# Kernel tuning notes

Measured on AMD Instinct MI355X. Metric: run time of the kernel, lower is better.

The kernel has to match this reference:

```python
import jax, jax.numpy as jnp
import numpy as np
from jax import lax

DIM = 192
HEADS = 6
WS = 8
SHIFT = 4
RED = max(8, DIM // 8)  # 24
HID = 4 * DIM


def _rel_index(ws):
    coords = np.stack(np.meshgrid(np.arange(ws), np.arange(ws), indexing='ij'))  # [2,ws,ws]
    flat = coords.reshape(2, -1)
    rel = (flat[:, :, None] - flat[:, None, :]).transpose(1, 2, 0)  # [T,T,2]
    rel[:, :, 0] += ws - 1
    rel[:, :, 1] += ws - 1
    rel[:, :, 0] *= 2 * ws - 1
    return rel.sum(-1)  # [T,T]


def _build_mask(h, w, ws, shift):
    img = np.zeros((h, w))
    slices = (slice(0, -ws), slice(-ws, -shift), slice(-shift, None))
    cnt = 0
    for hs in slices:
        for wcs in slices:
            img[hs, wcs] = cnt
            cnt += 1
    mw = img.reshape(h // ws, ws, w // ws, ws).transpose(0, 2, 1, 3).reshape(-1, ws * ws)
    diff = mw[:, None, :] - mw[:, :, None]  # [nW,T,T], diff[w,i,j]=mw[w,j]-mw[w,i]
    return np.where(diff != 0, -100.0, 0.0).astype(np.float32)


def _ln(x, g, b):
    m = x.mean(-1, keepdims=True)
    v = ((x - m) ** 2).mean(-1, keepdims=True)
    return (x - m) / jnp.sqrt(v + 1e-5) * g + b


def _conv(x, k, b, pad):
    y = lax.conv_general_dilated(x, k, (1, 1), [(pad, pad), (pad, pad)],
                                 dimension_numbers=('NCHW', 'OIHW', 'NCHW'))
    return y + b[None, :, None, None]


def setup_inputs() -> dict:
    key = jax.random.key(0)
    ks = jax.random.split(key, 16)
    rn = lambda k, s, sc=0.02: jax.random.normal(k, s, dtype=jnp.float32) * sc
    C = DIM
    return {
        'x': jax.random.normal(ks[0], (4, 256 * 256, C), dtype=jnp.float32),
        'ln1_g': jnp.ones((C,), jnp.float32), 'ln1_b': jnp.zeros((C,), jnp.float32),
        'w_qkv': rn(ks[1], (3 * C, C)), 'b_qkv': jnp.zeros((3 * C,), jnp.float32),
        'rel_table': rn(ks[2], ((2 * WS - 1) ** 2, HEADS)),
        'w_proj': rn(ks[3], (C, C)), 'b_proj': jnp.zeros((C,), jnp.float32),
        'ln2_g': jnp.ones((C,), jnp.float32), 'ln2_b': jnp.zeros((C,), jnp.float32),
        'w_fc1': rn(ks[4], (HID, C)), 'b_fc1': jnp.zeros((HID,), jnp.float32),
        'w_fc2': rn(ks[5], (C, HID)), 'b_fc2': jnp.zeros((C,), jnp.float32),
        'conv1_w': rn(ks[6], (RED, C, 1, 1)), 'conv1_b': jnp.zeros((RED,), jnp.float32),
        'conv2_w': rn(ks[7], (RED, RED, 3, 3)), 'conv2_b': jnp.zeros((RED,), jnp.float32),
        'conv3_w': rn(ks[8], (C, RED, 1, 1)), 'conv3_b': jnp.zeros((C,), jnp.float32),
        'se_w1': rn(ks[9], (RED, C)), 'se_w2': rn(ks[10], (C, RED)),
        'h': 256, 'w': 256,
    }


def reference(x, ln1_g, ln1_b, w_qkv, b_qkv, rel_table, w_proj, b_proj,
              ln2_g, ln2_b, w_fc1, b_fc1, w_fc2, b_fc2,
              conv1_w, conv1_b, conv2_w, conv2_b, conv3_w, conv3_b,
              se_w1, se_w2, h, w):
    B, _, C = x.shape
    ws, T, nh = WS, WS * WS, HEADS
    hd = C // nh
    scale = hd ** -0.5

    nx = _ln(x, ln1_g, ln1_b).reshape(B, h, w, C)
    local = nx.transpose(0, 3, 1, 2)  # NCHW for LCE

    # shifted window attention
    sh = jnp.roll(nx, (-SHIFT, -SHIFT), axis=(1, 2))
    win = sh.reshape(B, h // ws, ws, w // ws, ws, C).transpose(0, 1, 3, 2, 4, 5).reshape(-1, T, C)
    qkv = (win @ w_qkv.T + b_qkv).reshape(-1, T, 3, nh, hd).transpose(2, 0, 3, 1, 4)
    q, k, v = qkv[0] * scale, qkv[1], qkv[2]  # [BW, nh, T, hd]
    attn = jnp.einsum('whid,whjd->whij', q, k)  # [BW, nh, T, T]
    bias = rel_table[_rel_index(ws).reshape(-1)].reshape(T, T, nh).transpose(2, 0, 1)
    attn = attn + bias[None]
    mask = jnp.asarray(_build_mask(h, w, ws, SHIFT))  # [nW, T, T]
    nW = mask.shape[0]
    attn = attn.reshape(B, nW, nh, T, T) + mask[None, :, None]
    attn = jax.nn.softmax(attn, axis=-1).reshape(-1, nh, T, T)
    out = jnp.einsum('whij,whjd->whid', attn, v).transpose(0, 2, 1, 3).reshape(-1, T, C)
    out = out @ w_proj.T + b_proj
    out = out.reshape(B, h // ws, w // ws, ws, ws, C).transpose(0, 1, 3, 2, 4, 5).reshape(B, h, w, C)
    out = jnp.roll(out, (SHIFT, SHIFT), axis=(1, 2))

    x1 = x + out.reshape(B, h * w, C)
    n2 = _ln(x1, ln2_g, ln2_b)
    mlp = jax.nn.gelu(n2 @ w_fc1.T + b_fc1, approximate=False) @ w_fc2.T + b_fc2
    x2 = x1 + mlp

    # LocalContextExtractor (SE-style)
    y = _conv(local, conv1_w, conv1_b, 0)
    y = _conv(y, conv2_w, conv2_b, 1)
    y = _conv(y, conv3_w, conv3_b, 0)
    y = jnp.where(y >= 0, y, 0.2 * y)  # LeakyReLU(0.2)
    pooled = y.mean(axis=(2, 3))  # [B, C]
    wgt = jax.nn.sigmoid(jax.nn.relu(pooled @ se_w1.T) @ se_w2.T)
    y = y * wgt[:, :, None, None]
    lc = y.reshape(B, C, h * w).transpose(0, 2, 1)
    return x2 + lc
```

## Files before the change

kernel.cpp:

```cpp
#include <hip/hip_runtime.h>
#include <hip/hip_bf16.h>

typedef unsigned short u16;
typedef unsigned long long u64;
typedef __attribute__((ext_vector_type(8))) short short8x;
typedef __attribute__((ext_vector_type(4))) float f32x4;
typedef __bf16 bf16x8 __attribute__((ext_vector_type(8)));

#define SCALE 0.17677669529663687f

__device__ __forceinline__ u16 f2bf(float f) {
  unsigned u = __builtin_bit_cast(unsigned, f);
  unsigned r = (u + 0x7FFFu + ((u >> 16) & 1u)) >> 16;
  return (u16)r;
}
__device__ __forceinline__ float bf2f(u16 h) {
  return __builtin_bit_cast(float, ((unsigned)h) << 16);
}
__device__ __forceinline__ float gelu_f(float v) {
  float t = v * v;
  float a = __builtin_fmaf(t, -0.07135481627f, -1.59576912161f);
  float e = __expf(v * a);
  return v * __builtin_amdgcn_rcpf(1.0f + e);
}
__device__ __forceinline__ int swz(int row, int col, int ld) {
  return row * ld + ((((col >> 3) ^ (row & 7)) << 3) | (col & 7));
}
__device__ __forceinline__ short8x ldfrag(const u16* s, int row, int kb, int ld) {
  return *(const short8x*)(s + row * ld + (((kb >> 3) ^ (row & 7)) << 3));
}
__device__ __forceinline__ short8x ldg8(const u16* p) { return *(const short8x*)p; }

__device__ __forceinline__ f32x4 MFMA(short8x a, short8x b, f32x4 c) {
  return __builtin_amdgcn_mfma_f32_16x16x32_bf16(
      __builtin_bit_cast(bf16x8, a), __builtin_bit_cast(bf16x8, b), c, 0, 0, 0);
}
__device__ __forceinline__ u64 pack4(float a, float b, float c, float d) {
  return (u64)f2bf(a) | ((u64)f2bf(b) << 16) | ((u64)f2bf(c) << 32) | ((u64)f2bf(d) << 48);
}

__global__ void cvt_kernel(const float* __restrict__ wqkv, const float* __restrict__ wproj,
                           const float* __restrict__ wfc1, const float* __restrict__ wfc2,
                           const float* __restrict__ c1, const float* __restrict__ c3,
                           const float* __restrict__ c2,
                           u16* oq, u16* op, u16* o1, u16* o2, u16* oc1, u16* oc3,
                           float* ow2r) {
  int i = blockIdx.x * 256 + threadIdx.x;
  if (i < 110592) { float f = wqkv[i]; if (i < 36864) f *= SCALE; oq[i] = f2bf(f); return; }
  i -= 110592;
  if (i < 36864) { op[i] = f2bf(wproj[i]); return; }
  i -= 36864;
  if (i < 147456) { o1[i] = f2bf(wfc1[i]); return; }
  i -= 147456;
  if (i < 147456) { o2[i] = f2bf(wfc2[i]); return; }
  i -= 147456;
  if (i < 6144) { int r = i / 192, c = i - r * 192; oc1[i] = (r < 24) ? f2bf(c1[r * 192 + c]) : (u16)0; return; }
  i -= 6144;
  if (i < 6144) { int cc = i >> 5, k = i & 31; oc3[i] = (k < 24) ? f2bf(c3[cc * 24 + k]) : (u16)0; return; }
  i -= 6144;
  if (i < 5184) { int t = i / 576, rr = i - t * 576; int ci = rr / 24, co = rr - ci * 24;
                  ow2r[i] = c2[co * 216 + ci * 9 + t]; }
}

__global__ __launch_bounds__(256) void ln1_kernel(const float* __restrict__ x,
                                                  const float* __restrict__ g,
                                                  const float* __restrict__ b,
                                                  u16* __restrict__ nx) {
  const int wid = threadIdx.x >> 6, lane = threadIdx.x & 63;
  const int row = blockIdx.x * 4 + wid;
  const float* xr = x + row * 192;
  f32x4 v = {0.f, 0.f, 0.f, 0.f};
  if (lane < 48) v = *(const f32x4*)(xr + lane * 4);
  float s = v[0] + v[1] + v[2] + v[3];
  for (int m = 1; m < 64; m <<= 1) s += __shfl_xor(s, m);
  const float mean = s * (1.0f / 192.0f);
  f32x4 d;
#pragma unroll
  for (int r = 0; r < 4; ++r) d[r] = v[r] - mean;
  float q = (lane < 48) ? (d[0] * d[0] + d[1] * d[1] + d[2] * d[2] + d[3] * d[3]) : 0.f;
  for (int m = 1; m < 64; m <<= 1) q += __shfl_xor(q, m);
  const float rstd = rsqrtf(q * (1.0f / 192.0f) + 1e-5f);
  if (lane < 48) {
    const f32x4 gg = *(const f32x4*)(g + lane * 4);
    const f32x4 bb = *(const f32x4*)(b + lane * 4);
    u64 pk = pack4(d[0] * rstd * gg[0] + bb[0], d[1] * rstd * gg[1] + bb[1],
                   d[2] * rstd * gg[2] + bb[2], d[3] * rstd * gg[3] + bb[3]);
    *(u64*)(nx + row * 192 + lane * 4) = pk;
  }
}

__global__ __launch_bounds__(512, 4) void attn_kernel(
    const float* __restrict__ x, const u16* __restrict__ nx,
    const u16* __restrict__ wq, const float* __restrict__ bqkv,
    const float* __restrict__ rel, const u16* __restrict__ wp,
    const float* __restrict__ bproj, u16* __restrict__ vT,
    float* __restrict__ x1out) {
  __shared__ u16 sQK[64 * 384];
  __shared__ float sRel[1350];
  __shared__ int sG[64];

  const int tid = threadIdx.x, blk = blockIdx.x;
  const int b = blk >> 10, wi = (blk >> 5) & 31, wj = blk & 31;
  const int wv = tid >> 6, lane = tid & 63, lr = lane & 15, hi = lane >> 4;
  u16* vTw = vT + blk * 12288;

  for (int i = tid; i < 1350; i += 512) sRel[i] = rel[i];
  if (tid < 64) {
    int si = (wi * 8 + (tid >> 3) + 4) & 255, sj = (wj * 8 + (tid & 7) + 4) & 255;
    sG[tid] = b * 65536 + si * 256 + sj;
  }
  for (int i = tid; i < 64 * 96; i += 512) {
    int r = i / 96, w32 = i - r * 96;
    int si = (wi * 8 + (r >> 3) + 4) & 255, sj = (wj * 8 + (r & 7) + 4) & 255;
    int grow = b * 65536 + si * 256 + sj;
    unsigned v = ((const unsigned*)nx)[grow * 96 + w32];
    ((unsigned*)sQK)[r * 192 + ((((w32 >> 2) ^ (r & 7)) << 2) | (w32 & 3))] = v;
  }
  __syncthreads();

  f32x4 acc[4][4] = {};
  if (wv < 6) {
    const int wbase = wv * 64;
#pragma unroll
    for (int kk = 0; kk < 6; ++kk) {
      short8x Xf[4];
#pragma unroll
      for (int tt = 0; tt < 4; ++tt) Xf[tt] = ldfrag(sQK, tt * 16 + lr, kk * 32 + hi * 8, 384);
#pragma unroll
      for (int wt = 0; wt < 4; ++wt) {
        short8x Wf = ldg8(wq + (wbase + wt * 16 + lr) * 192 + kk * 32 + hi * 8);
#pragma unroll
        for (int tt = 0; tt < 4; ++tt) acc[wt][tt] = MFMA(Wf, Xf[tt], acc[wt][tt]);
      }
    }
  } else {
    const int vbase = (wv - 6) * 96;
#pragma unroll
    for (int half = 0; half < 2; ++half) {
      short8x Bf[3][6];
      float bv[3];
#pragma unroll
      for (int j = 0; j < 3; ++j) {
        const int vc = vbase + (half * 3 + j) * 16 + lr;
#pragma unroll
        for (int kk = 0; kk < 6; ++kk)
          Bf[j][kk] = ldg8(wq + (384 + vc) * 192 + kk * 32 + hi * 8);
        bv[j] = bqkv[384 + vc];
      }
#pragma unroll
      for (int mt = 0; mt < 4; ++mt) {
        f32x4 vacc[3] = {};
#pragma unroll
        for (int kk = 0; kk < 6; ++kk) {
          short8x A = ldfrag(sQK, mt * 16 + lr, kk * 32 + hi * 8, 384);
#pragma unroll
          for (int j = 0; j < 3; ++j) vacc[j] = MFMA(A, Bf[j][kk], vacc[j]);
        }
#pragma unroll
        for (int j = 0; j < 3; ++j) {
          u64 pk = pack4(vacc[j][0] + bv[j], vacc[j][1] + bv[j],
                         vacc[j][2] + bv[j], vacc[j][3] + bv[j]);
          *(u64*)(vTw + (vbase + (half * 3 + j) * 16 + lr) * 64 + mt * 16 + hi * 4) = pk;
        }
      }
    }
  }
  __syncthreads();

  if (wv < 6) {
    const int wbase = wv * 64;
#pragma unroll
    for (int wt = 0; wt < 4; ++wt) {
      const int oc0 = wbase + wt * 16 + hi * 4;
      const f32x4 bq = *(const f32x4*)(bqkv + oc0);
      const float sc = (oc0 < 192) ? SCALE : 1.0f;
#pragma unroll
      for (int tt = 0; tt < 4; ++tt) {
        u64 pk = pack4(acc[wt][tt][0] + bq[0] * sc, acc[wt][tt][1] + bq[1] * sc,
                       acc[wt][tt][2] + bq[2] * sc, acc[wt][tt][3] + bq[3] * sc);
        *(u64*)&sQK[swz(tt * 16 + lr, oc0, 384)] = pk;
      }
    }
  }
  __syncthreads();

  f32x4 S[3][4];
#pragma unroll
  for (int i = 0; i < 3; ++i) {
    const int s = wv + 8 * i, h3 = s >> 2, q = s & 3;
    short8x Aq = ldfrag(sQK, q * 16 + lr, h3 * 32 + hi * 8, 384);
#pragma unroll
    for (int nt = 0; nt < 4; ++nt) {
      short8x Bk = ldfrag(sQK, nt * 16 + lr, 192 + h3 * 32 + hi * 8, 384);
      S[i][nt] = MFMA(Aq, Bk, (f32x4){0.f, 0.f, 0.f, 0.f});
    }
#pragma unroll
    for (int r = 0; r < 4; ++r) {
      const int tI = q * 16 + hi * 4 + r;
      const int tri = tI >> 3, trj = tI & 7;
      const int ui = wi * 8 + tri, vi = wj * 8 + trj;
      const int rgi = (ui >= 248) + (ui >= 252), cgi = (vi >= 248) + (vi >= 252);
#pragma unroll
      for (int nt = 0; nt < 4; ++nt) {
        const int tJ = nt * 16 + lr;
        const int tci = tJ >> 3, tcj = tJ & 7;
        const int idx = (tri - tci + 7) * 15 + (trj - tcj + 7);
        float v = S[i][nt][r] + sRel[idx * 6 + h3];
        const int uj = wi * 8 + tci, vj = wj * 8 + tcj;
        const int rgj = (uj >= 248) + (uj >= 252), cgj = (vj >= 248) + (vj >= 252);
        if ((rgi != rgj) | (cgi != cgj)) v -= 100.0f;
        S[i][nt][r] = v;
      }
    }
#pragma unroll
    for (int r = 0; r < 4; ++r) {
      float mx = fmaxf(fmaxf(S[i][0][r], S[i][1][r]), fmaxf(S[i][2][r], S[i][3][r]));
      mx = fmaxf(mx, __shfl_xor(mx, 1));
      mx = fmaxf(mx, __shfl_xor(mx, 2));
      mx = fmaxf(mx, __shfl_xor(mx, 4));
      mx = fmaxf(mx, __shfl_xor(mx, 8));
      float sm = 0.f;
#pragma unroll
      for (int nt = 0; nt < 4; ++nt) { float e = __expf(S[i][nt][r] - mx); S[i][nt][r] = e; sm += e; }
      sm += __shfl_xor(sm, 1); sm += __shfl_xor(sm, 2);
      sm += __shfl_xor(sm, 4); sm += __shfl_xor(sm, 8);
      const float inv = 1.0f / sm;
#pragma unroll
      for (int nt = 0; nt < 4; ++nt) S[i][nt][r] *= inv;
    }
  }
  __syncthreads();

#pragma unroll
  for (int i = 0; i < 3; ++i) {
    const int s = wv + 8 * i, h3 = s >> 2, q = s & 3;
#pragma unroll
    for (int r = 0; r < 4; ++r)
#pragma unroll
      for (int nt = 0; nt < 4; ++nt)
        sQK[h3 * 4096 + swz(q * 16 + hi * 4 + r, nt * 16 + lr, 64)] = f2bf(S[i][nt][r]);
  }
  __syncthreads();

  f32x4 oacc[3][2] = {};
#pragma unroll
  for (int i = 0; i < 3; ++i) {
    const int t = wv + 8 * i, h3 = t >> 2, dt = (t >> 1) & 1, tth = t & 1;
#pragma unroll
    for (int kk = 0; kk < 2; ++kk) {
      short8x Va = ldg8(vTw + (h3 * 32 + dt * 16 + lr) * 64 + kk * 32 + hi * 8);
#pragma unroll
      for (int t2 = 0; t2 < 2; ++t2) {
        short8x Pf = ldfrag(sQK + h3 * 4096, tth * 32 + t2 * 16 + lr, kk * 32 + hi * 8, 64);
        oacc[i][t2] = MFMA(Va, Pf, oacc[i][t2]);
      }
    }
  }
  __syncthreads();

#pragma unroll
  for (int i = 0; i < 3; ++i) {
    const int t = wv + 8 * i, h3 = t >> 2, dt = (t >> 1) & 1, tth = t & 1;
#pragma unroll
    for (int t2 = 0; t2 < 2; ++t2) {
      u64 pk = pack4(oacc[i][t2][0], oacc[i][t2][1], oacc[i][t2][2], oacc[i][t2][3]);
      *(u64*)&sQK[swz(tth * 32 + t2 * 16 + lr, h3 * 32 + dt * 16 + hi * 4, 192)] = pk;
    }
  }
  __syncthreads();

  {
    const int nw = (wv < 4) ? 2 : 1;
    const int wt0 = (wv < 4) ? wv * 2 : (4 + wv);
    f32x4 pacc[2][4] = {};
#pragma unroll
    for (int kk = 0; kk < 6; ++kk) {
      short8x Of[4];
#pragma unroll
      for (int tt = 0; tt < 4; ++tt) Of[tt] = ldfrag(sQK, tt * 16 + lr, kk * 32 + hi * 8, 192);
      for (int w2 = 0; w2 < nw; ++w2) {
        short8x Wp = ldg8(wp + ((wt0 + w2) * 16 + lr) * 192 + kk * 32 + hi * 8);
#pragma unroll
        for (int tt = 0; tt < 4; ++tt) pacc[w2][tt] = MFMA(Wp, Of[tt], pacc[w2][tt]);
      }
    }
    for (int w2 = 0; w2 < nw; ++w2) {
      const int oc0 = (wt0 + w2) * 16 + hi * 4;
      const f32x4 bb = *(const f32x4*)(bproj + oc0);
#pragma unroll
      for (int tt = 0; tt < 4; ++tt) {
        const int grow = sG[tt * 16 + lr];
        const f32x4 xv = *(const f32x4*)(x + grow * 192 + oc0);
        f32x4 o;
#pragma unroll
        for (int r = 0; r < 4; ++r) o[r] = xv[r] + pacc[w2][tt][r] + bb[r];
        *(f32x4*)(x1out + grow * 192 + oc0) = o;
      }
    }
  }
}

__global__ __launch_bounds__(256) void conv1_kernel(const u16* __restrict__ nx,
                                                    const u16* __restrict__ w1,
                                                    const float* __restrict__ b1,
                                                    float* __restrict__ y1) {
  const int tid = threadIdx.x, wv = tid >> 6, lane = tid & 63, lr = lane & 15, hi = lane >> 4;
  const int g0 = blockIdx.x * 64;
  const int mt = wv;
  short8x Af[6];
#pragma unroll
  for (int kk = 0; kk < 6; ++kk)
    Af[kk] = ldg8(nx + (g0 + mt * 16 + lr) * 192 + kk * 32 + hi * 8);
  const int bI = g0 >> 16;
  const int hw0 = g0 & 65535;
#pragma unroll
  for (int nt = 0; nt < 2; ++nt) {
    f32x4 acc = {0.f, 0.f, 0.f, 0.f};
#pragma unroll
    for (int kk = 0; kk < 6; ++kk) {
      short8x Bf = ldg8(w1 + (nt * 16 + lr) * 192 + kk * 32 + hi * 8);
      acc = MFMA(Af[kk], Bf, acc);
    }
    const int c = nt * 16 + lr;
    if (c < 24) {
      const float bb = b1[c];
#pragma unroll
      for (int r = 0; r < 4; ++r) {
        const int pix = hw0 + mt * 16 + hi * 4 + r;
        y1[(bI * 24 + c) * 65536 + pix] = acc[r] + bb;
      }
    }
  }
}

__global__ __launch_bounds__(256) void conv2_kernel(const float* __restrict__ y1,
                                                    const float* __restrict__ w2r,
                                                    const float* __restrict__ cb2,
                                                    u16* __restrict__ y2) {
  const int j = threadIdx.x;
  const int i = blockIdx.x & 255;
  const int b = blockIdx.x >> 8;
  float acc[24];
#pragma unroll
  for (int r = 0; r < 24; ++r) acc[r] = cb2[r];
  const float* base = y1 + b * 24 * 65536;
  for (int t = 0; t < 9; ++t) {
    const int dh = t / 3 - 1, dw = t % 3 - 1;
    const int ii = i + dh, jj = j + dw;
    const bool ok = (ii >= 0) & (ii < 256) & (jj >= 0) & (jj < 256);
    const int offc = ok ? (ii * 256 + jj) : 0;
    const float* wt = w2r + t * 576;
    float v[24];
#pragma unroll
    for (int ci = 0; ci < 24; ++ci) {
      float vv = base[ci * 65536 + offc];
      v[ci] = ok ? vv : 0.0f;
    }
#pragma unroll
    for (int ci = 0; ci < 24; ++ci)
#pragma unroll
      for (int co = 0; co < 24; ++co)
        acc[co] += v[ci] * wt[ci * 24 + co];
  }
  u16* o = y2 + (b * 65536 + i * 256 + j) * 32;
#pragma unroll
  for (int r = 0; r < 24; ++r) o[r] = f2bf(acc[r]);
  ((unsigned long long*)(o + 24))[0] = 0ull;
  ((unsigned long long*)(o + 24))[1] = 0ull;
}

__global__ __launch_bounds__(256) void conv3_kernel(const u16* __restrict__ y2,
                                                    const u16* __restrict__ w3,
                                                    const float* __restrict__ b3,
                                                    u16* __restrict__ y,
                                                    float* __restrict__ pooled) {
  const int tid = threadIdx.x, wv = tid >> 6, lane = tid & 63, lr = lane & 15, hi = lane >> 4;
  const int g0 = blockIdx.x * 64;
  short8x Af[4];
#pragma unroll
  for (int mt = 0; mt < 4; ++mt)
    Af[mt] = ldg8(y2 + (g0 + mt * 16 + lr) * 32 + hi * 8);
  const int bI = g0 >> 16;
#pragma unroll
  for (int nt0 = 0; nt0 < 3; ++nt0) {
    const int c = (wv * 3 + nt0) * 16 + lr;
    short8x Bf = ldg8(w3 + c * 32 + hi * 8);
    const float bb = b3[c];
    float colsum = 0.f;
#pragma unroll
    for (int mt = 0; mt < 4; ++mt) {
      f32x4 acc = {0.f, 0.f, 0.f, 0.f};
      acc = MFMA(Af[mt], Bf, acc);
#pragma unroll
      for (int r = 0; r < 4; ++r) {
        float v = acc[r] + bb;
        v = (v >= 0.f) ? v : 0.2f * v;
        y[(g0 + mt * 16 + hi * 4 + r) * 192 + c] = f2bf(v);
        colsum += v;
      }
    }
    colsum += __shfl_xor(colsum, 16);
    colsum += __shfl_xor(colsum, 32);
    if (hi == 0) atomicAdd(&pooled[bI * 192 + c], colsum);
  }
}

__global__ void se_kernel(const float* __restrict__ pooled, const float* __restrict__ w1,
                          const float* __restrict__ w2, float* __restrict__ wgt) {
  __shared__ float t[24];
  const int b = blockIdx.x, lane = threadIdx.x;
  if (lane < 24) {
    float s = 0.f;
    for (int c = 0; c < 192; ++c) s += pooled[b * 192 + c] * (1.0f / 65536.0f) * w1[lane * 192 + c];
    t[lane] = fmaxf(s, 0.0f);
  }
  __syncthreads();
  for (int c = lane; c < 192; c += 64) {
    float s = 0.f;
#pragma unroll
    for (int r = 0; r < 24; ++r) s += t[r] * w2[c * 24 + r];
    wgt[b * 192 + c] = 1.0f / (1.0f + __expf(-s));
  }
}

__global__ __launch_bounds__(768, 6) void mlp_kernel(
    const float* x1, const float* __restrict__ g2, const float* __restrict__ b2,
    const u16* __restrict__ w1m, const float* __restrict__ bf1,
    const u16* __restrict__ w2m, const float* __restrict__ bf2,
    const u16* __restrict__ y, const float* __restrict__ wgt, float* out) {
  __shared__ u16 sN[64 * 192];
  __shared__ u16 sH[64 * 192];
  const int tid = threadIdx.x, wv = tid >> 6, lane = tid & 63, lr = lane & 15, hi = lane >> 4;
  const int g0 = blockIdx.x * 64;

  for (int row = wv; row < 64; row += 12) {
    const float* xr = x1 + (g0 + row) * 192;
    f32x4 v = {0.f, 0.f, 0.f, 0.f};
    if (lane < 48) v = *(const f32x4*)(xr + lane * 4);
    float s = v[0] + v[1] + v[2] + v[3];
    for (int m = 1; m < 64; m <<= 1) s += __shfl_xor(s, m);
    const float mean = s * (1.0f / 192.0f);
    f32x4 d;
#pragma unroll
    for (int r = 0; r < 4; ++r) d[r] = v[r] - mean;
    float q = (lane < 48) ? (d[0] * d[0] + d[1] * d[1] + d[2] * d[2] + d[3] * d[3]) : 0.f;
    for (int m = 1; m < 64; m <<= 1) q += __shfl_xor(q, m);
    const float rstd = rsqrtf(q * (1.0f / 192.0f) + 1e-5f);
    if (lane < 48) {
      const f32x4 gg = *(const f32x4*)(g2 + lane * 4);
      const f32x4 bb = *(const f32x4*)(b2 + lane * 4);
      u64 pk = pack4(d[0] * rstd * gg[0] + bb[0], d[1] * rstd * gg[1] + bb[1],
                     d[2] * rstd * gg[2] + bb[2], d[3] * rstd * gg[3] + bb[3]);
      *(u64*)&sN[swz(row, lane * 4, 192)] = pk;
    }
  }
  __syncthreads();

  f32x4 acc[4] = {};
  for (int c = 0; c < 4; ++c) {
    const int hcol = c * 192 + wv * 16 + lr;
    f32x4 a1[4] = {};
#pragma unroll
    for (int kk = 0; kk < 6; ++kk) {
      short8x B = ldg8(w1m + hcol * 192 + kk * 32 + hi * 8);
#pragma unroll
      for (int mt = 0; mt < 4; ++mt)
        a1[mt] = MFMA(ldfrag(sN, mt * 16 + lr, kk * 32 + hi * 8, 192), B, a1[mt]);
    }
    if (c) __syncthreads();
    const float bb1 = bf1[hcol];
#pragma unroll
    for (int mt = 0; mt < 4; ++mt)
#pragma unroll
      for (int r = 0; r < 4; ++r)
        sH[swz(mt * 16 + hi * 4 + r, wv * 16 + lr, 192)] = f2bf(gelu_f(a1[mt][r] + bb1));
    __syncthreads();
#pragma unroll
    for (int kk = 0; kk < 6; ++kk) {
      short8x B = ldg8(w2m + (wv * 16 + lr) * 768 + c * 192 + kk * 32 + hi * 8);
#pragma unroll
      for (int mt = 0; mt < 4; ++mt)
        acc[mt] = MFMA(ldfrag(sH, mt * 16 + lr, kk * 32 + hi * 8, 192), B, acc[mt]);
    }
  }

  const int bI = g0 >> 16;
  const int ocol = wv * 16 + lr;
  const float bb = bf2[ocol];
  const float wg = wgt[bI * 192 + ocol];
#pragma unroll
  for (int mt = 0; mt < 4; ++mt)
#pragma unroll
    for (int r = 0; r < 4; ++r) {
      const int grow = g0 + mt * 16 + hi * 4 + r;
      const float lc = bf2f(y[grow * 192 + ocol]) * wg;
      out[grow * 192 + ocol] = x1[grow * 192 + ocol] + acc[mt][r] + bb + lc;
    }
}

extern "C" void kernel_launch(void* const* d_in, const int* in_sizes, int n_in,
                              void* d_out, int out_size, void* d_ws, size_t ws_size,
                              hipStream_t stream) {
  const float* x     = (const float*)d_in[0];
  const float* ln1g  = (const float*)d_in[1];
  const float* ln1b  = (const float*)d_in[2];
  const float* wqkv  = (const float*)d_in[3];
  const float* bqkv  = (const float*)d_in[4];
  const float* rel   = (const float*)d_in[5];
  const float* wproj = (const float*)d_in[6];
  const float* bproj = (const float*)d_in[7];
  const float* ln2g  = (const float*)d_in[8];
  const float* ln2b  = (const float*)d_in[9];
  const float* wfc1  = (const float*)d_in[10];
  const float* bfc1  = (const float*)d_in[11];
  const float* wfc2  = (const float*)d_in[12];
  const float* bfc2  = (const float*)d_in[13];
  const float* c1w   = (const float*)d_in[14];
  const float* c1b   = (const float*)d_in[15];
  const float* c2w   = (const float*)d_in[16];
  const float* c2b   = (const float*)d_in[17];
  const float* c3w   = (const float*)d_in[18];
  const float* c3b   = (const float*)d_in[19];
  const float* sew1  = (const float*)d_in[20];
  const float* sew2  = (const float*)d_in[21];

  char* ws = (char*)d_ws;
  u16*   nx   = (u16*)(ws + 0);
  float* y1   = (float*)(ws + 100663296);
  u16*   y2   = (u16*)(ws + 125829120);
  u16*   yb   = (u16*)(ws + 142606336);
  u16*   wq   = (u16*)(ws + 243269632);
  u16*   wp   = (u16*)(ws + 243490816);
  u16*   w1m  = (u16*)(ws + 243564544);
  u16*   w2m  = (u16*)(ws + 243859456);
  u16*   cw1  = (u16*)(ws + 244154368);
  u16*   cw3  = (u16*)(ws + 244166656);
  float* w2r  = (float*)(ws + 244178944);
  float* pool = (float*)(ws + 244199680);
  float* wgt  = (float*)(ws + 244202752);
  float* out  = (float*)d_out;
  u16*   vT   = yb;

  hipMemsetAsync(pool, 0, 3072, stream);
  cvt_kernel<<<1797, 256, 0, stream>>>(wqkv, wproj, wfc1, wfc2, c1w, c3w, c2w,
                                       wq, wp, w1m, w2m, cw1, cw3, w2r);
  ln1_kernel<<<65536, 256, 0, stream>>>(x, ln1g, ln1b, nx);
  attn_kernel<<<4096, 512, 0, stream>>>(x, nx, wq, bqkv, rel, wp, bproj, vT, out);
  conv1_kernel<<<4096, 256, 0, stream>>>(nx, cw1, c1b, y1);
  conv2_kernel<<<1024, 256, 0, stream>>>(y1, w2r, c2b, y2);
  conv3_kernel<<<4096, 256, 0, stream>>>(y2, cw3, c3b, yb, pool);
  se_kernel<<<4, 64, 0, stream>>>(pool, sew1, sew2, wgt);
  mlp_kernel<<<4096, 768, 0, stream>>>(out, ln2g, ln2b, w1m, bfc1, w2m, bfc2, yb, wgt, out);
}
```

Before: 1.030 ms.

## Fuse LayerNorm1 and conv1 into the attention kernel, dropping the nx buffer

Removes the standalone ln1 and conv1 kernels. The attention kernel now computes LayerNorm on the fly from x for its 64 window pixels and writes the bf16 result straight into shared memory. It also computes the 1x1 conv1 from those shared-memory fragments during the QKV GEMM. This avoids writing and re-reading the 4x65536x192 bf16 nx buffer and saves two launches. In exchange the attention kernel gains extra registers and MFMA work, which could reduce occupancy.

```diff
diff --git a/kernel.cpp b/kernel.cpp
--- a/kernel.cpp
+++ b/kernel.cpp
@@ -62,39 +62,13 @@
                   ow2r[i] = c2[co * 216 + ci * 9 + t]; }
 }
 
-__global__ __launch_bounds__(256) void ln1_kernel(const float* __restrict__ x,
-                                                  const float* __restrict__ g,
-                                                  const float* __restrict__ b,
-                                                  u16* __restrict__ nx) {
-  const int wid = threadIdx.x >> 6, lane = threadIdx.x & 63;
-  const int row = blockIdx.x * 4 + wid;
-  const float* xr = x + row * 192;
-  f32x4 v = {0.f, 0.f, 0.f, 0.f};
-  if (lane < 48) v = *(const f32x4*)(xr + lane * 4);
-  float s = v[0] + v[1] + v[2] + v[3];
-  for (int m = 1; m < 64; m <<= 1) s += __shfl_xor(s, m);
-  const float mean = s * (1.0f / 192.0f);
-  f32x4 d;
-#pragma unroll
-  for (int r = 0; r < 4; ++r) d[r] = v[r] - mean;
-  float q = (lane < 48) ? (d[0] * d[0] + d[1] * d[1] + d[2] * d[2] + d[3] * d[3]) : 0.f;
-  for (int m = 1; m < 64; m <<= 1) q += __shfl_xor(q, m);
-  const float rstd = rsqrtf(q * (1.0f / 192.0f) + 1e-5f);
-  if (lane < 48) {
-    const f32x4 gg = *(const f32x4*)(g + lane * 4);
-    const f32x4 bb = *(const f32x4*)(b + lane * 4);
-    u64 pk = pack4(d[0] * rstd * gg[0] + bb[0], d[1] * rstd * gg[1] + bb[1],
-                   d[2] * rstd * gg[2] + bb[2], d[3] * rstd * gg[3] + bb[3]);
-    *(u64*)(nx + row * 192 + lane * 4) = pk;
-  }
-}
-
 __global__ __launch_bounds__(512, 4) void attn_kernel(
-    const float* __restrict__ x, const u16* __restrict__ nx,
-    const u16* __restrict__ wq, const float* __restrict__ bqkv,
-    const float* __restrict__ rel, const u16* __restrict__ wp,
-    const float* __restrict__ bproj, u16* __restrict__ vT,
-    float* __restrict__ x1out) {
+    const float* __restrict__ x, const float* __restrict__ g1,
+    const float* __restrict__ b1, const u16* __restrict__ wq,
+    const float* __restrict__ bqkv, const float* __restrict__ rel,
+    const u16* __restrict__ wp, const float* __restrict__ bproj,
+    const u16* __restrict__ w1, const float* __restrict__ cb1,
+    u16* __restrict__ vT, float* __restrict__ y1, float* __restrict__ x1out) {
   __shared__ u16 sQK[64 * 384];
   __shared__ float sRel[1350];
   __shared__ int sG[64];
@@ -109,16 +83,33 @@
     int si = (wi * 8 + (tid >> 3) + 4) & 255, sj = (wj * 8 + (tid & 7) + 4) & 255;
     sG[tid] = b * 65536 + si * 256 + sj;
   }
-  for (int i = tid; i < 64 * 96; i += 512) {
-    int r = i / 96, w32 = i - r * 96;
-    int si = (wi * 8 + (r >> 3) + 4) & 255, sj = (wj * 8 + (r & 7) + 4) & 255;
-    int grow = b * 65536 + si * 256 + sj;
-    unsigned v = ((const unsigned*)nx)[grow * 96 + w32];
-    ((unsigned*)sQK)[r * 192 + ((((w32 >> 2) ^ (r & 7)) << 2) | (w32 & 3))] = v;
+  for (int rr = 0; rr < 8; ++rr) {
+    const int r = wv * 8 + rr;
+    const int si = (wi * 8 + (r >> 3) + 4) & 255, sj = (wj * 8 + (r & 7) + 4) & 255;
+    const int grow = b * 65536 + si * 256 + sj;
+    f32x4 v = {0.f, 0.f, 0.f, 0.f};
+    if (lane < 48) v = *(const f32x4*)(x + grow * 192 + lane * 4);
+    float s = v[0] + v[1] + v[2] + v[3];
+    for (int m = 1; m < 64; m <<= 1) s += __shfl_xor(s, m);
+    const float mean = s * (1.0f / 192.0f);
+    f32x4 d;
+#pragma unroll
+    for (int t = 0; t < 4; ++t) d[t] = v[t] - mean;
+    float q = (lane < 48) ? (d[0] * d[0] + d[1] * d[1] + d[2] * d[2] + d[3] * d[3]) : 0.f;
+    for (int m = 1; m < 64; m <<= 1) q += __shfl_xor(q, m);
+    const float rstd = rsqrtf(q * (1.0f / 192.0f) + 1e-5f);
+    if (lane < 48) {
+      const f32x4 gg = *(const f32x4*)(g1 + lane * 4);
+      const f32x4 bb = *(const f32x4*)(b1 + lane * 4);
+      u64 pk = pack4(d[0] * rstd * gg[0] + bb[0], d[1] * rstd * gg[1] + bb[1],
+                     d[2] * rstd * gg[2] + bb[2], d[3] * rstd * gg[3] + bb[3]);
+      *(u64*)&sQK[swz(r, lane * 4, 384)] = pk;
+    }
   }
   __syncthreads();
 
   f32x4 acc[4][4] = {};
+  f32x4 c1a[2] = {};
   if (wv < 6) {
     const int wbase = wv * 64;
 #pragma unroll
@@ -131,6 +122,12 @@
         short8x Wf = ldg8(wq + (wbase + wt * 16 + lr) * 192 + kk * 32 + hi * 8);
 #pragma unroll
         for (int tt = 0; tt < 4; ++tt) acc[wt][tt] = MFMA(Wf, Xf[tt], acc[wt][tt]);
+      }
+      if (wv < 4) {
+        short8x W10 = ldg8(w1 + lr * 192 + kk * 32 + hi * 8);
+        short8x W11 = ldg8(w1 + (16 + lr) * 192 + kk * 32 + hi * 8);
+        c1a[0] = MFMA(Xf[wv], W10, c1a[0]);
+        c1a[1] = MFMA(Xf[wv], W11, c1a[1]);
       }
     }
   } else {
@@ -161,6 +158,20 @@
           u64 pk = pack4(vacc[j][0] + bv[j], vacc[j][1] + bv[j],
                          vacc[j][2] + bv[j], vacc[j][3] + bv[j]);
           *(u64*)(vTw + (vbase + (half * 3 + j) * 16 + lr) * 64 + mt * 16 + hi * 4) = pk;
+        }
+      }
+    }
+  }
+  if (wv < 4) {
+#pragma unroll
+    for (int nt = 0; nt < 2; ++nt) {
+      const int c = nt * 16 + lr;
+      if (c < 24) {
+        const float bb = cb1[c];
+#pragma unroll
+        for (int r = 0; r < 4; ++r) {
+          const int pix = sG[wv * 16 + hi * 4 + r] & 65535;
+          y1[(b * 24 + c) * 65536 + pix] = c1a[nt][r] + bb;
         }
       }
     }
@@ -295,39 +306,6 @@
 #pragma unroll
         for (int r = 0; r < 4; ++r) o[r] = xv[r] + pacc[w2][tt][r] + bb[r];
         *(f32x4*)(x1out + grow * 192 + oc0) = o;
-      }
-    }
-  }
-}
-
-__global__ __launch_bounds__(256) void conv1_kernel(const u16* __restrict__ nx,
-                                                    const u16* __restrict__ w1,
-                                                    const float* __restrict__ b1,
-                                                    float* __restrict__ y1) {
-  const int tid = threadIdx.x, wv = tid >> 6, lane = tid & 63, lr = lane & 15, hi = lane >> 4;
-  const int g0 = blockIdx.x * 64;
-  const int mt = wv;
-  short8x Af[6];
-#pragma unroll
-  for (int kk = 0; kk < 6; ++kk)
-    Af[kk] = ldg8(nx + (g0 + mt * 16 + lr) * 192 + kk * 32 + hi * 8);
-  const int bI = g0 >> 16;
-  const int hw0 = g0 & 65535;
-#pragma unroll
-  for (int nt = 0; nt < 2; ++nt) {
-    f32x4 acc = {0.f, 0.f, 0.f, 0.f};
-#pragma unroll
-    for (int kk = 0; kk < 6; ++kk) {
-      short8x Bf = ldg8(w1 + (nt * 16 + lr) * 192 + kk * 32 + hi * 8);
-      acc = MFMA(Af[kk], Bf, acc);
-    }
-    const int c = nt * 16 + lr;
-    if (c < 24) {
-      const float bb = b1[c];
-#pragma unroll
-      for (int r = 0; r < 4; ++r) {
-        const int pix = hw0 + mt * 16 + hi * 4 + r;
-        y1[(bI * 24 + c) * 65536 + pix] = acc[r] + bb;
       }
     }
   }
@@ -525,7 +503,6 @@
   const float* sew2  = (const float*)d_in[21];
 
   char* ws = (char*)d_ws;
-  u16*   nx   = (u16*)(ws + 0);
   float* y1   = (float*)(ws + 100663296);
   u16*   y2   = (u16*)(ws + 125829120);
   u16*   yb   = (u16*)(ws + 142606336);
@@ -544,9 +521,8 @@
   hipMemsetAsync(pool, 0, 3072, stream);
   cvt_kernel<<<1797, 256, 0, stream>>>(wqkv, wproj, wfc1, wfc2, c1w, c3w, c2w,
                                        wq, wp, w1m, w2m, cw1, cw3, w2r);
-  ln1_kernel<<<65536, 256, 0, stream>>>(x, ln1g, ln1b, nx);
-  attn_kernel<<<4096, 512, 0, stream>>>(x, nx, wq, bqkv, rel, wp, bproj, vT, out);
-  conv1_kernel<<<4096, 256, 0, stream>>>(nx, cw1, c1b, y1);
+  attn_kernel<<<4096, 512, 0, stream>>>(x, ln1g, ln1b, wq, bqkv, rel, wp, bproj,
+                                        cw1, c1b, vT, y1, out);
   conv2_kernel<<<1024, 256, 0, stream>>>(y1, w2r, c2b, y2);
   conv3_kernel<<<4096, 256, 0, stream>>>(y2, cw3, c3b, yb, pool);
   se_kernel<<<4, 64, 0, stream>>>(pool, sew1, sew2, wgt);
```

After: 1.107 ms. 7.5% more time.
